# Performance work log

Hardware: AMD Instinct MI355X
Metric: run time of the kernel (lower is better)

## Reference

```python
import jax, jax.numpy as jnp
import numpy as np

INPUT_DIM, HIDDEN, HEADS = 310, 64, 8
WINDOW, PERIOD = 5, 3
NEG_INF = -jnp.inf


def _masks(seq_len):
    i = jnp.arange(seq_len)[:, None]
    j = jnp.arange(seq_len)[None, :]
    local = jnp.abs(i - j) <= WINDOW
    sparse = (j % PERIOD == 0) | (i == j)
    to_add = lambda m: jnp.where(m, 0.0, NEG_INF).astype(jnp.float32)
    return to_add(local), to_add(sparse)


def _mha(xp, in_w, in_b, out_w, out_b, mask):
    # xp: [B,S,E]; in_w: [3E,E]; out_w: [E,E]; mask: [S,S] additive
    B, S, E = xp.shape
    d = E // HEADS
    qkv = xp @ in_w.T + in_b                      # [B,S,3E]
    q, k, v = jnp.split(qkv, 3, axis=-1)
    split_heads = lambda t: t.reshape(B, S, HEADS, d).transpose(0, 2, 1, 3)
    q, k, v = split_heads(q), split_heads(k), split_heads(v)
    scores = jnp.einsum('bhqd,bhkd->bhqk', q, k) / jnp.sqrt(jnp.float32(d))
    scores = scores + mask                         # broadcast [S,S]
    attn = jax.nn.softmax(scores, axis=-1)
    o = jnp.einsum('bhqk,bhkd->bhqd', attn, v)
    o = o.transpose(0, 2, 1, 3).reshape(B, S, E)
    return o @ out_w.T + out_b


def setup_inputs() -> dict:
    key = jax.random.key(0)
    ks = jax.random.split(key, 16)
    E = HIDDEN
    s = lambda fan: 1.0 / np.sqrt(fan)
    u = lambda k, shape, fan: jax.random.uniform(k, shape, jnp.float32, -s(fan), s(fan))
    return {
        'x': jax.random.normal(ks[0], (16, 1024, INPUT_DIM), jnp.float32),
        'proj_w': u(ks[1], (E, INPUT_DIM), INPUT_DIM),
        'proj_b': u(ks[2], (E,), INPUT_DIM),
        'loc_in_w': u(ks[3], (3 * E, E), E),
        'loc_in_b': jnp.zeros((3 * E,), jnp.float32),
        'loc_out_w': u(ks[4], (E, E), E),
        'loc_out_b': jnp.zeros((E,), jnp.float32),
        'glob_in_w': u(ks[5], (3 * E, E), E),
        'glob_in_b': jnp.zeros((3 * E,), jnp.float32),
        'glob_out_w': u(ks[6], (E, E), E),
        'glob_out_b': jnp.zeros((E,), jnp.float32),
        'fusion_w': u(ks[7], (E, 2 * E), 2 * E),
        'fusion_b': u(ks[8], (E,), 2 * E),
        'pool_w1': u(ks[9], (E // 2, E), E),
        'pool_b1': u(ks[10], (E // 2,), E),
        'pool_w2': u(ks[11], (1, E // 2), E // 2),
        'pool_b2': u(ks[12], (1,), E // 2),
    }


def reference(x, proj_w, proj_b, loc_in_w, loc_in_b, loc_out_w, loc_out_b,
              glob_in_w, glob_in_b, glob_out_w, glob_out_b,
              fusion_w, fusion_b, pool_w1, pool_b1, pool_w2, pool_b2):
    B, S, _ = x.shape
    local_mask, sparse_mask = _masks(S)
    xp = x @ proj_w.T + proj_b                     # [B,S,E]
    local_out = _mha(xp, loc_in_w, loc_in_b, loc_out_w, loc_out_b, local_mask)
    global_out = _mha(xp, glob_in_w, glob_in_b, glob_out_w, glob_out_b, sparse_mask)
    fused = jnp.concatenate([local_out, global_out], axis=-1) @ fusion_w.T + fusion_b
    scores = jnp.tanh(fused @ pool_w1.T + pool_b1) @ pool_w2.T + pool_b2  # [B,S,1]
    w = jax.nn.softmax(scores, axis=1)             # softmax over seq dim
    return jnp.sum(fused * w, axis=1)              # [B,E]
```

## Files before the change

### kernel.cpp

```cpp
#include <hip/hip_runtime.h>
#include <hip/hip_bf16.h>


typedef __attribute__((ext_vector_type(8))) short short8;
typedef __attribute__((ext_vector_type(4))) float float4v;

#define INV_SQRT8 0.3535533905932738f

__device__ __forceinline__ float4 ld4(const float* p) { return *(const float4*)p; }

__device__ __forceinline__ float4 f4fma(float s, float4 w, float4 a) {
  a.x = fmaf(s, w.x, a.x); a.y = fmaf(s, w.y, a.y);
  a.z = fmaf(s, w.z, a.z); a.w = fmaf(s, w.w, a.w);
  return a;
}

__device__ __forceinline__ short f2bf(float x) {
  __hip_bfloat16 b = __float2bfloat16(x);
  unsigned short u; __builtin_memcpy(&u, &b, 2);
  return (short)u;
}
__device__ __forceinline__ float bf2f(short s) {
  return __uint_as_float(((unsigned)(unsigned short)s) << 16);
}
__device__ __forceinline__ void bsplit(float x, short& h, short& l) {
  h = f2bf(x);
  l = f2bf(x - bf2f(h));
}

__global__ __launch_bounds__(256) void prep_w(
    const float* __restrict__ pw, const float* __restrict__ liw,
    const float* __restrict__ giw, const float* __restrict__ fw,
    const float* __restrict__ low, const float* __restrict__ gow,
    const float* __restrict__ lob, const float* __restrict__ gob,
    const float* __restrict__ fb,
    short* __restrict__ wb, float* __restrict__ bc, float* __restrict__ numden,
    short* __restrict__ VTh, short* __restrict__ VTl)
{
  unsigned idx = blockIdx.x * 256 + threadIdx.x;
  if (idx < 53248u) {
    float v; unsigned ho, lo_;
    if (idx < 20480u) {
      unsigned r = idx / 320u, k = idx - r * 320u;
      v = (k < 310u) ? pw[r * 310u + k] : 0.f;
      ho = 0u + idx; lo_ = 20480u + idx;
    } else if (idx < 32768u) {
      unsigned i = idx - 20480u; v = liw[i]; ho = 40960u + i; lo_ = 53248u + i;
    } else if (idx < 45056u) {
      unsigned i = idx - 32768u; v = giw[i]; ho = 65536u + i; lo_ = 77824u + i;
    } else {
      unsigned i = idx - 45056u;
      unsigned n = i >> 7, k = i & 127u;
      float s = 0.f;
      if (k < 64u) {
        for (int e = 0; e < 64; e++) s += fw[n * 128 + e] * low[e * 64 + k];
      } else {
        for (int e = 0; e < 64; e++) s += fw[n * 128 + 64 + e] * gow[e * 64 + (k - 64u)];
      }
      v = s; ho = 90112u + i; lo_ = 98304u + i;
    }
    short h, l; bsplit(v, h, l);
    wb[ho] = h; wb[lo_] = l;
    if (idx < 64u) {
      float b = fb[idx];
      for (int e = 0; e < 64; e++)
        b += lob[e] * fw[idx * 128 + e] + gob[e] * fw[idx * 128 + 64 + e];
      bc[idx] = b;
    }
    if (idx < 1041u) numden[idx] = 0.f;
  } else {
    unsigned t = idx - 53248u;
    if (t < 370688u) {
      unsigned pos; short hv = 0;
      if (t < 360448u) {
        unsigned bh = t / 2816u;
        unsigned rem = t - bh * 2816u;
        unsigned n8 = rem / 352u;
        unsigned kk = rem - n8 * 352u;
        pos = (bh * 16u + 8u + n8) * 352u + kk;
        if (n8 == 0u) hv = (short)0x3F80;
      } else {
        unsigned t2 = t - 360448u;
        unsigned bh = t2 / 80u;
        unsigned rem = t2 - bh * 80u;
        unsigned n = rem / 10u;
        unsigned kk = 342u + (rem - n * 10u);
        pos = (bh * 16u + n) * 352u + kk;
      }
      VTh[pos] = hv; VTl[pos] = 0;
    }
  }
}

__global__ __launch_bounds__(256) void gemm_proj_qkv(
    const float* __restrict__ X,
    const short* __restrict__ PWh, const short* __restrict__ PWl,
    const float* __restrict__ pb,
    const short* __restrict__ LWh, const short* __restrict__ LWl,
    const short* __restrict__ GWh, const short* __restrict__ GWl,
    const float* __restrict__ lb, const float* __restrict__ gb,
    float* __restrict__ qkv_l, float* __restrict__ qkv_g,
    short* __restrict__ KH, short* __restrict__ KL,
    short* __restrict__ VTh, short* __restrict__ VTl)
{
  __shared__ __align__(16) short XPH[64][72];
  __shared__ __align__(16) short XPL[64][72];
  const int lane = threadIdx.x & 63;
  const int w = threadIdx.x >> 6;
  const int q = lane >> 4, r = lane & 15;
  const int mloc = w * 16;
  const int m0 = blockIdx.x * 64 + mloc;

  float4v accp[4];
  #pragma unroll
  for (int g = 0; g < 4; g++) {
    float bv = pb[g * 16 + r];
    float4v t = {bv, bv, bv, bv};
    accp[g] = t;
  }
  const float* arow = X + (size_t)(m0 + r) * 310;
  #pragma unroll
  for (int ks = 0; ks < 10; ks++) {
    const int k0 = ks * 32 + q * 8;
    float av[8];
    if (ks < 9) {
      const float* ap = arow + k0;
      #pragma unroll
      for (int t = 0; t < 4; t++) {
        float2 f = *(const float2*)(ap + t * 2);
        av[t*2] = f.x; av[t*2+1] = f.y;
      }
    } else {
      #pragma unroll
      for (int j = 0; j < 8; j++) {
        int kidx = k0 + j;
        av[j] = (kidx < 310) ? arow[kidx] : 0.f;
      }
    }
    short8 ah, al;
    #pragma unroll
    for (int i = 0; i < 8; i++) { short h, l; bsplit(av[i], h, l); ah[i]=h; al[i]=l; }
    #pragma unroll
    for (int g = 0; g < 4; g++) {
      short8 bh = *(const short8*)(PWh + (size_t)(g * 16 + r) * 320 + k0);
      short8 bl = *(const short8*)(PWl + (size_t)(g * 16 + r) * 320 + k0);
      accp[g] = __builtin_amdgcn_mfma_f32_16x16x32_bf16(al, bh, accp[g], 0, 0, 0);
      accp[g] = __builtin_amdgcn_mfma_f32_16x16x32_bf16(ah, bl, accp[g], 0, 0, 0);
      accp[g] = __builtin_amdgcn_mfma_f32_16x16x32_bf16(ah, bh, accp[g], 0, 0, 0);
    }
  }
  #pragma unroll
  for (int g = 0; g < 4; g++)
    #pragma unroll
    for (int e = 0; e < 4; e++) {
      short h, l; bsplit(accp[g][e], h, l);
      XPH[mloc + q * 4 + e][g * 16 + r] = h;
      XPL[mloc + q * 4 + e][g * 16 + r] = l;
    }

  float4v acc[2][12];
  #pragma unroll
  for (int nf = 0; nf < 12; nf++) {
    float bv0 = lb[nf * 16 + r], bv1 = gb[nf * 16 + r];
    float4v t0 = {bv0, bv0, bv0, bv0};
    float4v t1 = {bv1, bv1, bv1, bv1};
    acc[0][nf] = t0; acc[1][nf] = t1;
  }
  #pragma unroll
  for (int ks = 0; ks < 2; ks++) {
    const int k0 = ks * 32 + q * 8;
    short8 ah = *(const short8*)&XPH[mloc + r][k0];
    short8 al = *(const short8*)&XPL[mloc + r][k0];
    #pragma unroll
    for (int nf = 0; nf < 12; nf++) {
      short8 bh0 = *(const short8*)(LWh + (size_t)(nf * 16 + r) * 64 + k0);
      short8 bl0 = *(const short8*)(LWl + (size_t)(nf * 16 + r) * 64 + k0);
      acc[0][nf] = __builtin_amdgcn_mfma_f32_16x16x32_bf16(al, bh0, acc[0][nf], 0, 0, 0);
      acc[0][nf] = __builtin_amdgcn_mfma_f32_16x16x32_bf16(ah, bl0, acc[0][nf], 0, 0, 0);
      acc[0][nf] = __builtin_amdgcn_mfma_f32_16x16x32_bf16(ah, bh0, acc[0][nf], 0, 0, 0);
      short8 bh1 = *(const short8*)(GWh + (size_t)(nf * 16 + r) * 64 + k0);
      short8 bl1 = *(const short8*)(GWl + (size_t)(nf * 16 + r) * 64 + k0);
      acc[1][nf] = __builtin_amdgcn_mfma_f32_16x16x32_bf16(al, bh1, acc[1][nf], 0, 0, 0);
      acc[1][nf] = __builtin_amdgcn_mfma_f32_16x16x32_bf16(ah, bl1, acc[1][nf], 0, 0, 0);
      acc[1][nf] = __builtin_amdgcn_mfma_f32_16x16x32_bf16(ah, bh1, acc[1][nf], 0, 0, 0);
    }
  }

  const int b = m0 >> 10;
  const int bh8 = b * 8;
  #pragma unroll
  for (int e = 0; e < 4; e++) {
    const int row = m0 + q * 4 + e;
    const int i = row & 1023;
    #pragma unroll
    for (int nf = 0; nf < 12; nf++) {
      qkv_l[(size_t)row * 192 + nf * 16 + r] = acc[0][nf][e];
      qkv_g[(size_t)row * 192 + nf * 16 + r] = acc[1][nf][e];
    }
    if (i % 3 == 0) {
      const int kk = i / 3;
      #pragma unroll
      for (int nf = 4; nf < 12; nf++) {
        const int col = nf * 16 + r;
        float v = acc[1][nf][e];
        short h, l; bsplit(v, h, l);
        if (col < 128) {
          const int ck = col - 64;
          const int hh = ck >> 3, d = ck & 7;
          KH[(size_t)(bh8 + hh) * 2816 + kk * 8 + d] = h;
          KL[(size_t)(bh8 + hh) * 2816 + kk * 8 + d] = l;
        } else {
          const int cv = col - 128;
          const int hh = cv >> 3, d = cv & 7;
          VTh[((size_t)(bh8 + hh) * 16 + d) * 352 + kk] = h;
          VTl[((size_t)(bh8 + hh) * 16 + d) * 352 + kk] = l;
        }
      }
    }
  }
}

__global__ __launch_bounds__(256) void attn(
    const float* __restrict__ qkv_g, const float* __restrict__ qkv_l,
    const short* __restrict__ KH, const short* __restrict__ KL,
    const short* __restrict__ VTh, const short* __restrict__ VTl,
    float* __restrict__ o_g, float* __restrict__ pl, float* __restrict__ o_l)
{
  __shared__ short Pbuf[4][2][2][16][32];
  const int u = blockIdx.x;
  if (u < 2048) {
    const int qt = u & 15, h = (u >> 4) & 7, b = u >> 7;
    const int w = threadIdx.x >> 6, lane = threadIdx.x & 63;
    const int quad = lane >> 4, r = lane & 15;
    const int bh = b * 8 + h;
    const int m0 = qt * 64 + w * 16;

    const short8 z8 = {0,0,0,0,0,0,0,0};
    short8 qh = z8, ql = z8;
    if (quad == 0) {
      const float* qp = qkv_g + (size_t)(b * 1024 + m0 + r) * 192 + h * 8;
      float4 a0 = ld4(qp), a1 = ld4(qp + 4);
      float qv[8] = {a0.x, a0.y, a0.z, a0.w, a1.x, a1.y, a1.z, a1.w};
      #pragma unroll
      for (int d = 0; d < 8; d++) { short hh, ll; bsplit(qv[d], hh, ll); qh[d]=hh; ql[d]=ll; }
    }
    const short* kbase  = KH + (size_t)bh * 2816;
    const short* klbase = KL + (size_t)bh * 2816;
    const short* vhbase = VTh + ((size_t)bh * 16 + r) * 352;
    const short* vlbase = VTl + ((size_t)bh * 16 + r) * 352;

    float4v oacc = {0.f, 0.f, 0.f, 0.f};
    short8 vprev_h = z8, vprev_l = z8;

    for (int kc = 0; kc < 11; kc++) {
      short8 vh = *(const short8*)(vhbase + kc * 32 + quad * 8);
      short8 vl = *(const short8*)(vlbase + kc * 32 + quad * 8);

      short8 pA = z8, pB = z8;
      if (kc > 0) {
        pA = *(const short8*)&Pbuf[w][(kc - 1) & 1][0][r][quad * 8];
        pB = *(const short8*)&Pbuf[w][(kc - 1) & 1][1][r][quad * 8];
      }

      short8 kh0 = z8, kl0 = z8, kh1 = z8, kl1 = z8;
      if (quad == 0) {
        kh0 = *(const short8*)(kbase  + (size_t)(kc * 32 + r) * 8);
        kl0 = *(const short8*)(klbase + (size_t)(kc * 32 + r) * 8);
        kh1 = *(const short8*)(kbase  + (size_t)(kc * 32 + 16 + r) * 8);
        kl1 = *(const short8*)(klbase + (size_t)(kc * 32 + 16 + r) * 8);
      }
      float4v s0 = {0.f,0.f,0.f,0.f}, s1 = {0.f,0.f,0.f,0.f};
      s0 = __builtin_amdgcn_mfma_f32_16x16x32_bf16(qh, kl0, s0, 0, 0, 0);
      s0 = __builtin_amdgcn_mfma_f32_16x16x32_bf16(ql, kh0, s0, 0, 0, 0);
      s0 = __builtin_amdgcn_mfma_f32_16x16x32_bf16(qh, kh0, s0, 0, 0, 0);
      s1 = __builtin_amdgcn_mfma_f32_16x16x32_bf16(qh, kl1, s1, 0, 0, 0);
      s1 = __builtin_amdgcn_mfma_f32_16x16x32_bf16(ql, kh1, s1, 0, 0, 0);
      s1 = __builtin_amdgcn_mfma_f32_16x16x32_bf16(qh, kh1, s1, 0, 0, 0);

      if (kc > 0) {
        oacc = __builtin_amdgcn_mfma_f32_16x16x32_bf16(pA, vprev_l, oacc, 0, 0, 0);
        oacc = __builtin_amdgcn_mfma_f32_16x16x32_bf16(pB, vprev_h, oacc, 0, 0, 0);
        oacc = __builtin_amdgcn_mfma_f32_16x16x32_bf16(pA, vprev_h, oacc, 0, 0, 0);
      }

      const int par = kc & 1;
      const int key0 = kc * 32 + r, key1 = key0 + 16;
      #pragma unroll
      for (int e = 0; e < 4; e++) {
        float p0 = (key0 < 342) ? __expf(s0[e] * INV_SQRT8) : 0.f;
        float p1 = (key1 < 342) ? __expf(s1[e] * INV_SQRT8) : 0.f;
        short h0, l0, h1, l1; bsplit(p0, h0, l0); bsplit(p1, h1, l1);
        const int qloc = quad * 4 + e;
        Pbuf[w][par][0][qloc][r]      = h0;
        Pbuf[w][par][0][qloc][16 + r] = h1;
        Pbuf[w][par][1][qloc][r]      = l0;
        Pbuf[w][par][1][qloc][16 + r] = l1;
      }
      vprev_h = vh; vprev_l = vl;
    }
    {
      short8 pA = *(const short8*)&Pbuf[w][0][0][r][quad * 8];
      short8 pB = *(const short8*)&Pbuf[w][0][1][r][quad * 8];
      oacc = __builtin_amdgcn_mfma_f32_16x16x32_bf16(pA, vprev_l, oacc, 0, 0, 0);
      oacc = __builtin_amdgcn_mfma_f32_16x16x32_bf16(pB, vprev_h, oacc, 0, 0, 0);
      oacc = __builtin_amdgcn_mfma_f32_16x16x32_bf16(pA, vprev_h, oacc, 0, 0, 0);
    }

    #pragma unroll
    for (int e = 0; e < 4; e++) {
      const int orow = b * 1024 + m0 + quad * 4 + e;
      if (r < 8)       o_g[(size_t)orow * 64 + h * 8 + r] = oacc[e];
      else if (r == 8) pl[(size_t)orow * 8 + h] = oacc[e];
    }
  } else {
    int t = (u - 2048) * 256 + threadIdx.x;
    int h = t & 7;
    int i = (t >> 3) & 1023;
    int b = t >> 13;
    const float* base = qkv_l + (size_t)b * 1024 * 192;
    const float* qp = base + (size_t)i * 192 + h * 8;
    float4 q0 = ld4(qp), q1 = ld4(qp + 4);
    float l = 0.f;
    float4 o0 = make_float4(0.f, 0.f, 0.f, 0.f);
    float4 o1 = make_float4(0.f, 0.f, 0.f, 0.f);
    int jlo = i - 5; if (jlo < 0) jlo = 0;
    int jhi = i + 5; if (jhi > 1023) jhi = 1023;
    for (int j = jlo; j <= jhi; j++) {
      const float* kp = base + (size_t)j * 192 + 64 + h * 8;
      float4 k0 = ld4(kp), k1 = ld4(kp + 4);
      float s = q0.x * k0.x + q0.y * k0.y + q0.z * k0.z + q0.w * k0.w
              + q1.x * k1.x + q1.y * k1.y + q1.z * k1.z + q1.w * k1.w;
      float p = __expf(s * INV_SQRT8);
      l += p;
      float4 v0 = ld4(kp + 64), v1 = ld4(kp + 68);
      o0 = f4fma(p, v0, o0);
      o1 = f4fma(p, v1, o1);
    }
    float inv = 1.f / l;
    float* op = o_l + (size_t)(b * 1024 + i) * 64 + h * 8;
    float4 r0, r1;
    r0.x = o0.x * inv; r0.y = o0.y * inv; r0.z = o0.z * inv; r0.w = o0.w * inv;
    r1.x = o1.x * inv; r1.y = o1.y * inv; r1.z = o1.z * inv; r1.w = o1.w * inv;
    *(float4*)op = r0;
    *(float4*)(op + 4) = r1;
  }
}

__global__ __launch_bounds__(256) void gemm_fuse_score(
    const float* __restrict__ o_l, const float* __restrict__ o_g,
    const float* __restrict__ pl, const float* __restrict__ qkv_g,
    const short* __restrict__ Wh, const short* __restrict__ Wl,
    const float* __restrict__ bc,
    const float* __restrict__ pw1, const float* __restrict__ pb1,
    const float* __restrict__ pw2, const float* __restrict__ pb2,
    float* __restrict__ num, float* __restrict__ den,
    unsigned* __restrict__ cnt, float* __restrict__ out)
{
  __shared__ float Ls[64][68];
  __shared__ float partial[4][64];
  __shared__ unsigned lastflag;
  const int tid = threadIdx.x;
  const int lane = tid & 63, w = tid >> 6;
  const int quad = lane >> 4, r = lane & 15;
  const int bx = blockIdx.x;
  const int m0 = bx * 64 + w * 16;

  float4v acc[4];
  #pragma unroll
  for (int g = 0; g < 4; g++) {
    float bv = bc[g * 16 + r];
    float4v t = {bv, bv, bv, bv};
    acc[g] = t;
  }

  #pragma unroll
  for (int ks = 0; ks < 4; ks++) {
    const int k0 = ks * 32 + quad * 8;
    const int row = m0 + r;
    float av[8];
    if (ks < 2) {
      const float* ap = o_l + (size_t)row * 64 + k0;
      float4 f0 = ld4(ap), f1 = ld4(ap + 4);
      av[0]=f0.x; av[1]=f0.y; av[2]=f0.z; av[3]=f0.w;
      av[4]=f1.x; av[5]=f1.y; av[6]=f1.z; av[7]=f1.w;
    } else {
      const int off = k0 - 64;
      const int h = off >> 3;
      const float* op = o_g + (size_t)row * 64 + off;
      float4 O0 = ld4(op), O1 = ld4(op + 4);
      float l = pl[(size_t)row * 8 + h];
      const int i = row & 1023;
      if (i % 3 != 0) {
        const float* base = qkv_g + (size_t)row * 192;
        const float* qp = base + h * 8;
        const float* kpp = base + 64 + h * 8;
        const float* vp = base + 128 + h * 8;
        float4 q0 = ld4(qp), q1 = ld4(qp + 4);
        float4 k0v = ld4(kpp), k1v = ld4(kpp + 4);
        float s = q0.x*k0v.x + q0.y*k0v.y + q0.z*k0v.z + q0.w*k0v.w
                + q1.x*k1v.x + q1.y*k1v.y + q1.z*k1v.z + q1.w*k1v.w;
        float p = __expf(s * INV_SQRT8);
        float4 v0 = ld4(vp), v1 = ld4(vp + 4);
        O0 = f4fma(p, v0, O0); O1 = f4fma(p, v1, O1);
        l += p;
      }
      float inv = 1.f / l;
      av[0]=O0.x*inv; av[1]=O0.y*inv; av[2]=O0.z*inv; av[3]=O0.w*inv;
      av[4]=O1.x*inv; av[5]=O1.y*inv; av[6]=O1.z*inv; av[7]=O1.w*inv;
    }
    short8 ah, al;
    #pragma unroll
    for (int i2 = 0; i2 < 8; i2++) { short h2, l2; bsplit(av[i2], h2, l2); ah[i2]=h2; al[i2]=l2; }
    #pragma unroll
    for (int g = 0; g < 4; g++) {
      short8 bh = *(const short8*)(Wh + (size_t)(g * 16 + r) * 128 + k0);
      short8 bl = *(const short8*)(Wl + (size_t)(g * 16 + r) * 128 + k0);
      acc[g] = __builtin_amdgcn_mfma_f32_16x16x32_bf16(al, bh, acc[g], 0, 0, 0);
      acc[g] = __builtin_amdgcn_mfma_f32_16x16x32_bf16(ah, bl, acc[g], 0, 0, 0);
      acc[g] = __builtin_amdgcn_mfma_f32_16x16x32_bf16(ah, bh, acc[g], 0, 0, 0);
    }
  }

  #pragma unroll
  for (int g = 0; g < 4; g++)
    #pragma unroll
    for (int e = 0; e < 4; e++)
      Ls[w * 16 + quad * 4 + e][g * 16 + r] = acc[g][e];
  __syncthreads();

  float4 fr[16];
  #pragma unroll
  for (int e = 0; e < 16; e++) fr[e] = *(float4*)&Ls[lane][e * 4];

  float psc = 0.f;
  #pragma unroll
  for (int jj = 0; jj < 8; jj++) {
    const int j = w * 8 + jj;
    const float* wr = pw1 + j * 64;
    float hj = pb1[j];
    #pragma unroll
    for (int e = 0; e < 16; e++) {
      float4 wv = ld4(wr + e * 4);
      hj += fr[e].x * wv.x + fr[e].y * wv.y + fr[e].z * wv.z + fr[e].w * wv.w;
    }
    float e2 = __expf(2.f * hj);
    psc += ((e2 - 1.f) / (e2 + 1.f)) * pw2[j];
  }
  partial[w][lane] = psc;
  __syncthreads();
  if (w == 0) {
    const int b = bx >> 4;
    float sc = pb2[0] + partial[0][lane] + partial[1][lane]
             + partial[2][lane] + partial[3][lane];
    float p = __expf(sc);
    #pragma unroll
    for (int e = 0; e < 16; e++) {
      Ls[lane][e*4+0] = p * fr[e].x; Ls[lane][e*4+1] = p * fr[e].y;
      Ls[lane][e*4+2] = p * fr[e].z; Ls[lane][e*4+3] = p * fr[e].w;
    }
    float colsum = 0.f;
    #pragma unroll 8
    for (int s = 0; s < 64; s++) colsum += Ls[s][lane];
    atomicAdd(&num[b * 64 + lane], colsum);
    float ps = p;
    #pragma unroll
    for (int off = 32; off > 0; off >>= 1)
      ps += __shfl_xor(ps, off, 64);
    if (lane == 0) atomicAdd(&den[b], ps);
  }

  if (tid == 0) {
    __threadfence();
    lastflag = (atomicAdd(cnt, 1u) == 255u) ? 1u : 0u;
  }
  __syncthreads();
  if (lastflag) {
    __threadfence();
    for (int k = tid; k < 1024; k += 256) {
      float nv = __hip_atomic_load(&num[k], __ATOMIC_RELAXED, __HIP_MEMORY_SCOPE_AGENT);
      float dv = __hip_atomic_load(&den[k >> 6], __ATOMIC_RELAXED, __HIP_MEMORY_SCOPE_AGENT);
      out[k] = nv / dv;
    }
  }
}

extern "C" void kernel_launch(void* const* d_in, const int* in_sizes, int n_in,
                              void* d_out, int out_size, void* d_ws, size_t ws_size,
                              hipStream_t stream)
{
  const float* x          = (const float*)d_in[0];
  const float* proj_w     = (const float*)d_in[1];
  const float* proj_b     = (const float*)d_in[2];
  const float* loc_in_w   = (const float*)d_in[3];
  const float* loc_in_b   = (const float*)d_in[4];
  const float* loc_out_w  = (const float*)d_in[5];
  const float* loc_out_b  = (const float*)d_in[6];
  const float* glob_in_w  = (const float*)d_in[7];
  const float* glob_in_b  = (const float*)d_in[8];
  const float* glob_out_w = (const float*)d_in[9];
  const float* glob_out_b = (const float*)d_in[10];
  const float* fusion_w   = (const float*)d_in[11];
  const float* fusion_b   = (const float*)d_in[12];
  const float* pw1        = (const float*)d_in[13];
  const float* pb1        = (const float*)d_in[14];
  const float* pw2        = (const float*)d_in[15];
  const float* pb2        = (const float*)d_in[16];

  float* ws = (float*)d_ws;
  float* qkv_g = ws;
  float* qkv_l = ws + 4587520;
  float* o_l   = ws + 7733248;
  float* o_g   = ws + 8781824;
  float* pl    = ws + 9830400;
  short* KH    = (short*)(ws + 9961472);
  short* KL    = (short*)(ws + 10141696);
  short* VTh   = (short*)(ws + 10321920);
  short* VTl   = (short*)(ws + 10682368);
  float* bc    = ws + 11042816;
  float* numden= ws + 11042880;
  float* num   = numden;
  float* den   = numden + 1024;
  unsigned* cnt= (unsigned*)(numden + 1040);
  short* wb    = (short*)(ws + 11043921);
  short* projh = wb;           short* projl = wb + 20480;
  short* linh  = wb + 40960;   short* linl  = wb + 53248;
  short* ginh  = wb + 65536;   short* ginl  = wb + 77824;
  short* wfh   = wb + 90112;   short* wfl   = wb + 98304;
  float* out   = (float*)d_out;

  dim3 blk(256);
  prep_w<<<1656, blk, 0, stream>>>(proj_w, loc_in_w, glob_in_w, fusion_w,
                                   loc_out_w, glob_out_w, loc_out_b, glob_out_b,
                                   fusion_b, wb, bc, numden, VTh, VTl);
  gemm_proj_qkv<<<256, blk, 0, stream>>>(
      x, projh, projl, proj_b, linh, linl, ginh, ginl, loc_in_b, glob_in_b,
      qkv_l, qkv_g, KH, KL, VTh, VTl);
  attn<<<2560, blk, 0, stream>>>(qkv_g, qkv_l, KH, KL, VTh, VTl, o_g, pl, o_l);
  gemm_fuse_score<<<256, blk, 0, stream>>>(
      o_l, o_g, pl, qkv_g, wfh, wfl, bc, pw1, pb1, pw2, pb2, num, den, cnt, out);
}
```

Before: 180.4 us.

## Split projection/QKV and fusion GEMMs across more blocks with finer wave partitioning

gemm_proj_qkv now gives each block 16 rows instead of 64. The four waves split the projection's output columns, share the result through LDS, and then split the local/global QKV GEMMs by branch and column half. gemm_fuse_score likewise handles 32 rows per block, with waves split by row tile and column pair. The aim is to fill the 256 CUs with 1024 and 512 blocks instead of 256, and to cut per-thread accumulator registers. The cost is redundant weight loads per block, extra syncs, and twice as many atomics in the final reduction.

Measured after the change: 183.2 us. No clear change (+1.6%).

```diff
diff --git a/kernel.cpp b/kernel.cpp
--- a/kernel.cpp
+++ b/kernel.cpp
@@ -103,20 +103,18 @@
     short* __restrict__ KH, short* __restrict__ KL,
     short* __restrict__ VTh, short* __restrict__ VTl)
 {
-  __shared__ __align__(16) short XPH[64][72];
-  __shared__ __align__(16) short XPL[64][72];
+  __shared__ __align__(16) short XPH[16][72];
+  __shared__ __align__(16) short XPL[16][72];
   const int lane = threadIdx.x & 63;
   const int w = threadIdx.x >> 6;
   const int q = lane >> 4, r = lane & 15;
-  const int mloc = w * 16;
-  const int m0 = blockIdx.x * 64 + mloc;
-
-  float4v accp[4];
-  #pragma unroll
-  for (int g = 0; g < 4; g++) {
-    float bv = pb[g * 16 + r];
+  const int m0 = blockIdx.x * 16;
+
+  float4v accp;
+  {
+    float bv = pb[w * 16 + r];
     float4v t = {bv, bv, bv, bv};
-    accp[g] = t;
+    accp = t;
   }
   const float* arow = X + (size_t)(m0 + r) * 310;
   #pragma unroll
@@ -140,49 +138,46 @@
     short8 ah, al;
     #pragma unroll
     for (int i = 0; i < 8; i++) { short h, l; bsplit(av[i], h, l); ah[i]=h; al[i]=l; }
-    #pragma unroll
-    for (int g = 0; g < 4; g++) {
-      short8 bh = *(const short8*)(PWh + (size_t)(g * 16 + r) * 320 + k0);
-      short8 bl = *(const short8*)(PWl + (size_t)(g * 16 + r) * 320 + k0);
-      accp[g] = __builtin_amdgcn_mfma_f32_16x16x32_bf16(al, bh, accp[g], 0, 0, 0);
-      accp[g] = __builtin_amdgcn_mfma_f32_16x16x32_bf16(ah, bl, accp[g], 0, 0, 0);
-      accp[g] = __builtin_amdgcn_mfma_f32_16x16x32_bf16(ah, bh, accp[g], 0, 0, 0);
-    }
-  }
-  #pragma unroll
-  for (int g = 0; g < 4; g++)
-    #pragma unroll
-    for (int e = 0; e < 4; e++) {
-      short h, l; bsplit(accp[g][e], h, l);
-      XPH[mloc + q * 4 + e][g * 16 + r] = h;
-      XPL[mloc + q * 4 + e][g * 16 + r] = l;
-    }
-
-  float4v acc[2][12];
-  #pragma unroll
-  for (int nf = 0; nf < 12; nf++) {
-    float bv0 = lb[nf * 16 + r], bv1 = gb[nf * 16 + r];
-    float4v t0 = {bv0, bv0, bv0, bv0};
-    float4v t1 = {bv1, bv1, bv1, bv1};
-    acc[0][nf] = t0; acc[1][nf] = t1;
+    short8 bh = *(const short8*)(PWh + (size_t)(w * 16 + r) * 320 + k0);
+    short8 bl = *(const short8*)(PWl + (size_t)(w * 16 + r) * 320 + k0);
+    accp = __builtin_amdgcn_mfma_f32_16x16x32_bf16(al, bh, accp, 0, 0, 0);
+    accp = __builtin_amdgcn_mfma_f32_16x16x32_bf16(ah, bl, accp, 0, 0, 0);
+    accp = __builtin_amdgcn_mfma_f32_16x16x32_bf16(ah, bh, accp, 0, 0, 0);
+  }
+  #pragma unroll
+  for (int e = 0; e < 4; e++) {
+    short h, l; bsplit(accp[e], h, l);
+    XPH[q * 4 + e][w * 16 + r] = h;
+    XPL[q * 4 + e][w * 16 + r] = l;
+  }
+  __syncthreads();
+
+  const int br = w >> 1, hf = w & 1;
+  const short* Wh = br ? GWh : LWh;
+  const short* Wl = br ? GWl : LWl;
+  const float* bb = br ? gb : lb;
+  float* qkv = br ? qkv_g : qkv_l;
+
+  float4v acc[6];
+  #pragma unroll
+  for (int j = 0; j < 6; j++) {
+    float bv = bb[(hf * 6 + j) * 16 + r];
+    float4v t = {bv, bv, bv, bv};
+    acc[j] = t;
   }
   #pragma unroll
   for (int ks = 0; ks < 2; ks++) {
     const int k0 = ks * 32 + q * 8;
-    short8 ah = *(const short8*)&XPH[mloc + r][k0];
-    short8 al = *(const short8*)&XPL[mloc + r][k0];
-    #pragma unroll
-    for (int nf = 0; nf < 12; nf++) {
-      short8 bh0 = *(const short8*)(LWh + (size_t)(nf * 16 + r) * 64 + k0);
-      short8 bl0 = *(const short8*)(LWl + (size_t)(nf * 16 + r) * 64 + k0);
-      acc[0][nf] = __builtin_amdgcn_mfma_f32_16x16x32_bf16(al, bh0, acc[0][nf], 0, 0, 0);
-      acc[0][nf] = __builtin_amdgcn_mfma_f32_16x16x32_bf16(ah, bl0, acc[0][nf], 0, 0, 0);
-      acc[0][nf] = __builtin_amdgcn_mfma_f32_16x16x32_bf16(ah, bh0, acc[0][nf], 0, 0, 0);
-      short8 bh1 = *(const short8*)(GWh + (size_t)(nf * 16 + r) * 64 + k0);
-      short8 bl1 = *(const short8*)(GWl + (size_t)(nf * 16 + r) * 64 + k0);
-      acc[1][nf] = __builtin_amdgcn_mfma_f32_16x16x32_bf16(al, bh1, acc[1][nf], 0, 0, 0);
-      acc[1][nf] = __builtin_amdgcn_mfma_f32_16x16x32_bf16(ah, bl1, acc[1][nf], 0, 0, 0);
-      acc[1][nf] = __builtin_amdgcn_mfma_f32_16x16x32_bf16(ah, bh1, acc[1][nf], 0, 0, 0);
+    short8 ah = *(const short8*)&XPH[r][k0];
+    short8 al = *(const short8*)&XPL[r][k0];
+    #pragma unroll
+    for (int j = 0; j < 6; j++) {
+      const int nf = hf * 6 + j;
+      short8 bh = *(const short8*)(Wh + (size_t)(nf * 16 + r) * 64 + k0);
+      short8 bl = *(const short8*)(Wl + (size_t)(nf * 16 + r) * 64 + k0);
+      acc[j] = __builtin_amdgcn_mfma_f32_16x16x32_bf16(al, bh, acc[j], 0, 0, 0);
+      acc[j] = __builtin_amdgcn_mfma_f32_16x16x32_bf16(ah, bl, acc[j], 0, 0, 0);
+      acc[j] = __builtin_amdgcn_mfma_f32_16x16x32_bf16(ah, bh, acc[j], 0, 0, 0);
     }
   }
 
@@ -193,27 +188,30 @@
     const int row = m0 + q * 4 + e;
     const int i = row & 1023;
     #pragma unroll
-    for (int nf = 0; nf < 12; nf++) {
-      qkv_l[(size_t)row * 192 + nf * 16 + r] = acc[0][nf][e];
-      qkv_g[(size_t)row * 192 + nf * 16 + r] = acc[1][nf][e];
-    }
-    if (i % 3 == 0) {
+    for (int j = 0; j < 6; j++) {
+      const int nf = hf * 6 + j;
+      qkv[(size_t)row * 192 + nf * 16 + r] = acc[j][e];
+    }
+    if (br == 1 && i % 3 == 0) {
       const int kk = i / 3;
       #pragma unroll
-      for (int nf = 4; nf < 12; nf++) {
-        const int col = nf * 16 + r;
-        float v = acc[1][nf][e];
-        short h, l; bsplit(v, h, l);
-        if (col < 128) {
-          const int ck = col - 64;
-          const int hh = ck >> 3, d = ck & 7;
-          KH[(size_t)(bh8 + hh) * 2816 + kk * 8 + d] = h;
-          KL[(size_t)(bh8 + hh) * 2816 + kk * 8 + d] = l;
-        } else {
-          const int cv = col - 128;
-          const int hh = cv >> 3, d = cv & 7;
-          VTh[((size_t)(bh8 + hh) * 16 + d) * 352 + kk] = h;
-          VTl[((size_t)(bh8 + hh) * 16 + d) * 352 + kk] = l;
+      for (int j = 0; j < 6; j++) {
+        const int nf = hf * 6 + j;
+        if (nf >= 4) {
+          const int col = nf * 16 + r;
+          float v = acc[j][e];
+          short h, l; bsplit(v, h, l);
+          if (col < 128) {
+            const int ck = col - 64;
+            const int hh = ck >> 3, d = ck & 7;
+            KH[(size_t)(bh8 + hh) * 2816 + kk * 8 + d] = h;
+            KL[(size_t)(bh8 + hh) * 2816 + kk * 8 + d] = l;
+          } else {
+            const int cv = col - 128;
+            const int hh = cv >> 3, d = cv & 7;
+            VTh[((size_t)(bh8 + hh) * 16 + d) * 352 + kk] = h;
+            VTl[((size_t)(bh8 + hh) * 16 + d) * 352 + kk] = l;
+          }
         }
       }
     }
@@ -356,21 +354,22 @@
     float* __restrict__ num, float* __restrict__ den,
     unsigned* __restrict__ cnt, float* __restrict__ out)
 {
-  __shared__ float Ls[64][68];
+  __shared__ float Ls[32][68];
   __shared__ float partial[4][64];
   __shared__ unsigned lastflag;
   const int tid = threadIdx.x;
   const int lane = tid & 63, w = tid >> 6;
   const int quad = lane >> 4, r = lane & 15;
   const int bx = blockIdx.x;
-  const int m0 = bx * 64 + w * 16;
-
-  float4v acc[4];
-  #pragma unroll
-  for (int g = 0; g < 4; g++) {
-    float bv = bc[g * 16 + r];
-    float4v t = {bv, bv, bv, bv};
-    acc[g] = t;
+  const int t = w >> 1, p = w & 1;
+  const int m0 = bx * 32 + t * 16;
+
+  float4v acc[2];
+  #pragma unroll
+  for (int gg = 0; gg < 2; gg++) {
+    float bv = bc[(p * 2 + gg) * 16 + r];
+    float4v tv = {bv, bv, bv, bv};
+    acc[gg] = tv;
   }
 
   #pragma unroll
@@ -399,10 +398,10 @@
         float4 k0v = ld4(kpp), k1v = ld4(kpp + 4);
         float s = q0.x*k0v.x + q0.y*k0v.y + q0.z*k0v.z + q0.w*k0v.w
                 + q1.x*k1v.x + q1.y*k1v.y + q1.z*k1v.z + q1.w*k1v.w;
-        float p = __expf(s * INV_SQRT8);
+        float pd = __expf(s * INV_SQRT8);
         float4 v0 = ld4(vp), v1 = ld4(vp + 4);
-        O0 = f4fma(p, v0, O0); O1 = f4fma(p, v1, O1);
-        l += p;
+        O0 = f4fma(pd, v0, O0); O1 = f4fma(pd, v1, O1);
+        l += pd;
       }
       float inv = 1.f / l;
       av[0]=O0.x*inv; av[1]=O0.y*inv; av[2]=O0.z*inv; av[3]=O0.w*inv;
@@ -412,30 +411,32 @@
     #pragma unroll
     for (int i2 = 0; i2 < 8; i2++) { short h2, l2; bsplit(av[i2], h2, l2); ah[i2]=h2; al[i2]=l2; }
     #pragma unroll
-    for (int g = 0; g < 4; g++) {
+    for (int gg = 0; gg < 2; gg++) {
+      const int g = p * 2 + gg;
       short8 bh = *(const short8*)(Wh + (size_t)(g * 16 + r) * 128 + k0);
       short8 bl = *(const short8*)(Wl + (size_t)(g * 16 + r) * 128 + k0);
-      acc[g] = __builtin_amdgcn_mfma_f32_16x16x32_bf16(al, bh, acc[g], 0, 0, 0);
-      acc[g] = __builtin_amdgcn_mfma_f32_16x16x32_bf16(ah, bl, acc[g], 0, 0, 0);
-      acc[g] = __builtin_amdgcn_mfma_f32_16x16x32_bf16(ah, bh, acc[g], 0, 0, 0);
-    }
-  }
-
-  #pragma unroll
-  for (int g = 0; g < 4; g++)
+      acc[gg] = __builtin_amdgcn_mfma_f32_16x16x32_bf16(al, bh, acc[gg], 0, 0, 0);
+      acc[gg] = __builtin_amdgcn_mfma_f32_16x16x32_bf16(ah, bl, acc[gg], 0, 0, 0);
+      acc[gg] = __builtin_amdgcn_mfma_f32_16x16x32_bf16(ah, bh, acc[gg], 0, 0, 0);
+    }
+  }
+
+  #pragma unroll
+  for (int gg = 0; gg < 2; gg++)
     #pragma unroll
     for (int e = 0; e < 4; e++)
-      Ls[w * 16 + quad * 4 + e][g * 16 + r] = acc[g][e];
+      Ls[t * 16 + quad * 4 + e][(p * 2 + gg) * 16 + r] = acc[gg][e];
   __syncthreads();
 
+  const int row31 = lane & 31, half = lane >> 5;
   float4 fr[16];
   #pragma unroll
-  for (int e = 0; e < 16; e++) fr[e] = *(float4*)&Ls[lane][e * 4];
+  for (int e = 0; e < 16; e++) fr[e] = *(float4*)&Ls[row31][e * 4];
 
   float psc = 0.f;
   #pragma unroll
-  for (int jj = 0; jj < 8; jj++) {
-    const int j = w * 8 + jj;
+  for (int jj = 0; jj < 4; jj++) {
+    const int j = w * 8 + half * 4 + jj;
     const float* wr = pw1 + j * 64;
     float hj = pb1[j];
     #pragma unroll
@@ -449,20 +450,25 @@
   partial[w][lane] = psc;
   __syncthreads();
   if (w == 0) {
-    const int b = bx >> 4;
-    float sc = pb2[0] + partial[0][lane] + partial[1][lane]
-             + partial[2][lane] + partial[3][lane];
-    float p = __expf(sc);
-    #pragma unroll
-    for (int e = 0; e < 16; e++) {
-      Ls[lane][e*4+0] = p * fr[e].x; Ls[lane][e*4+1] = p * fr[e].y;
-      Ls[lane][e*4+2] = p * fr[e].z; Ls[lane][e*4+3] = p * fr[e].w;
+    const int b = bx >> 5;
+    float pv = 0.f;
+    if (lane < 32) {
+      float sc = pb2[0];
+      #pragma unroll
+      for (int w2 = 0; w2 < 4; w2++)
+        sc += partial[w2][lane] + partial[w2][lane + 32];
+      pv = __expf(sc);
+      #pragma unroll
+      for (int e = 0; e < 16; e++) {
+        Ls[lane][e*4+0] = pv * fr[e].x; Ls[lane][e*4+1] = pv * fr[e].y;
+        Ls[lane][e*4+2] = pv * fr[e].z; Ls[lane][e*4+3] = pv * fr[e].w;
+      }
     }
     float colsum = 0.f;
     #pragma unroll 8
-    for (int s = 0; s < 64; s++) colsum += Ls[s][lane];
+    for (int s = 0; s < 32; s++) colsum += Ls[s][lane];
     atomicAdd(&num[b * 64 + lane], colsum);
-    float ps = p;
+    float ps = pv;
     #pragma unroll
     for (int off = 32; off > 0; off >>= 1)
       ps += __shfl_xor(ps, off, 64);
@@ -471,7 +477,7 @@
 
   if (tid == 0) {
     __threadfence();
-    lastflag = (atomicAdd(cnt, 1u) == 255u) ? 1u : 0u;
+    lastflag = (atomicAdd(cnt, 1u) == 511u) ? 1u : 0u;
   }
   __syncthreads();
   if (lastflag) {
@@ -532,10 +538,10 @@
   prep_w<<<1656, blk, 0, stream>>>(proj_w, loc_in_w, glob_in_w, fusion_w,
                                    loc_out_w, glob_out_w, loc_out_b, glob_out_b,
                                    fusion_b, wb, bc, numden, VTh, VTl);
-  gemm_proj_qkv<<<256, blk, 0, stream>>>(
+  gemm_proj_qkv<<<1024, blk, 0, stream>>>(
       x, projh, projl, proj_b, linh, linl, ginh, ginl, loc_in_b, glob_in_b,
       qkv_l, qkv_g, KH, KL, VTh, VTl);
   attn<<<2560, blk, 0, stream>>>(qkv_g, qkv_l, KH, KL, VTh, VTl, o_g, pl, o_l);
-  gemm_fuse_score<<<256, blk, 0, stream>>>(
+  gemm_fuse_score<<<512, blk, 0, stream>>>(
       o_l, o_g, pl, qkv_g, wfh, wfl, bc, pw1, pb1, pw2, pb2, num, den, cnt, out);
 }
```
